# Performance work log

Hardware: AMD Instinct MI355X
Metric: run time of the kernel (lower is better)

Reference implementation:

```python
import jax, jax.numpy as jnp
import numpy as np

B, S, D, K = 64, 2048, 192, 128  # batch, seq, projection_dim, memoryBankSize


def setup_inputs() -> dict:
    key = jax.random.key(0)
    k1, k2, k3 = jax.random.split(key, 3)
    return {
        "projections": jax.random.normal(k1, (B, S, D), jnp.float32),
        "mem_bank": jax.random.normal(k2, (K, D), jnp.float32),
        "glu_w": jax.random.normal(k3, (D, 2 * D), jnp.float32) * 0.05,
        "glu_b": jnp.zeros((2 * D,), jnp.float32),
    }


def _l2_normalize(x, axis):
    # matches tf.math.l2_normalize (eps inside the max under the sqrt)
    sq = jnp.sum(x * x, axis=axis, keepdims=True)
    return x / jnp.sqrt(jnp.maximum(sq, 1e-12))


def _sinkhorn(out):
    # out: [K, N] cosine similarities
    Q = jnp.exp(out / 0.05)
    Kf = jnp.asarray(Q.shape[0], Q.dtype)
    Bf = jnp.asarray(Q.shape[1], Q.dtype)
    Q = Q / jnp.sum(Q)
    for _ in range(3):  # fixed 3 iterations, as in source
        Q = Q / (jnp.sum(Q, axis=1, keepdims=True) * Kf)  # row normalize
        Q = Q / (jnp.sum(Q, axis=0, keepdims=True) * Bf)  # col normalize
    return Q * Bf


def reference(projections, mem_bank, glu_w, glu_b):
    Bsz, Ssz, Dd = projections.shape
    x = projections.reshape(-1, Dd)                      # [N, D]
    proj_n = _l2_normalize(x, axis=1)                    # [N, D]
    mem_n = _l2_normalize(mem_bank, axis=1)              # [K, D]
    sim = jnp.einsum('kd,nd->kn', mem_n, proj_n)         # [K, N]
    Q = _sinkhorn(sim)                                   # [K, N]
    # top_k(Q^T, 1) per token == argmax over codebook axis
    idx = jnp.argmax(Q, axis=0)                          # [N] int
    assign = mem_bank[idx]                               # gather, [N, D]
    # GLU: Dense(2D) then value * sigmoid(gate)
    lin = assign @ glu_w + glu_b                         # [N, 2D]
    gated = lin[:, :Dd] * jax.nn.sigmoid(lin[:, Dd:])    # [N, D]
    # reduce_mean over the stacked pair == average
    return (projections + gated.reshape(Bsz, Ssz, Dd)) * 0.5
```

## Files before the change

kernel.cpp:

```cpp
#include <hip/hip_runtime.h>

#define NTOK  131072
#define DDIM  192
#define KMEM  128
#define TWOD  384
#define NBLK  1024

typedef _Float16 half8 __attribute__((ext_vector_type(8)));
typedef float   floatx4 __attribute__((ext_vector_type(4)));

__global__ __launch_bounds__(192) void prep_kernel(
    const float* __restrict__ mb, const float* __restrict__ W,
    const float* __restrict__ bias, _Float16* __restrict__ bhi,
    _Float16* __restrict__ blo, float* __restrict__ tab) {
  __shared__ float row[DDIM];
  __shared__ float red[DDIM];
  __shared__ float s_rn;
  const int k = blockIdx.x;
  const int t = threadIdx.x;
  float m = mb[k * DDIM + t];
  row[t] = m;
  red[t] = m * m;
  __syncthreads();
  if (t == 0) {
    float s = 0.f;
    for (int i = 0; i < DDIM; ++i) s += red[i];
    s_rn = 1.0f / sqrtf(fmaxf(s, 1e-12f));
  }
  __syncthreads();
  const float mn = m * s_rn;
  const _Float16 hh = (_Float16)mn;
  const float lo = (mn - (float)hh) * 4096.0f;
  bhi[k * DDIM + t] = hh;
  blo[k * DDIM + t] = (_Float16)lo;
  float a = bias[t], g = bias[DDIM + t];
  for (int d = 0; d < DDIM; ++d) {
    float r = row[d];
    a = fmaf(r, W[d * TWOD + t], a);
    g = fmaf(r, W[d * TWOD + DDIM + t], g);
  }
  float sg = 1.0f / (1.0f + expf(-g));
  tab[k * DDIM + t] = a * sg;
}

#define LSTR 40
__global__ __launch_bounds__(256, 2) void sim_kernel(
    const float* __restrict__ proj, const _Float16* __restrict__ bhi_g,
    const _Float16* __restrict__ blo_g, float* __restrict__ E,
    double* __restrict__ RpT) {
  __shared__ _Float16 Ahi[128 * LSTR];
  __shared__ _Float16 Alo[128 * LSTR];
  __shared__ _Float16 Bhi[128 * LSTR];
  __shared__ _Float16 Blo[128 * LSTR];
  __shared__ float rn_s[128];
  __shared__ float red[4][64];
  const int tid = threadIdx.x;
  const int lane = tid & 63;
  const int wid = tid >> 6;
  const int tok_half = wid & 1;
  const int code_half = wid >> 1;
  const long n0 = (long)blockIdx.x * 128;
  const int st_tok = tid >> 1;
  const int st_h = tid & 1;

  floatx4 acc1[4][4];
  floatx4 acc2[4][4];
#pragma unroll
  for (int i = 0; i < 4; ++i)
#pragma unroll
    for (int j = 0; j < 4; ++j) {
      acc1[i][j] = (floatx4)0.0f;
      acc2[i][j] = (floatx4)0.0f;
    }
  float nsq = 0.f;

  const int m_row = lane & 15;
  const int quad = lane >> 4;
  const int kcol = quad * 8;

  for (int c = 0; c < 6; ++c) {
    {
      const float* src = &proj[(n0 + st_tok) * DDIM + c * 32 + st_h * 16];
      float4 p0 = *(const float4*)(src + 0);
      float4 p1 = *(const float4*)(src + 4);
      float4 p2 = *(const float4*)(src + 8);
      float4 p3 = *(const float4*)(src + 12);
      float xs[16] = {p0.x, p0.y, p0.z, p0.w, p1.x, p1.y, p1.z, p1.w,
                      p2.x, p2.y, p2.z, p2.w, p3.x, p3.y, p3.z, p3.w};
      half8 h0, h1, l0, l1;
#pragma unroll
      for (int i = 0; i < 8; ++i) {
        float x = xs[i];
        nsq = fmaf(x, x, nsq);
        _Float16 hh = (_Float16)x;
        h0[i] = hh;
        l0[i] = (_Float16)((x - (float)hh) * 4096.0f);
      }
#pragma unroll
      for (int i = 0; i < 8; ++i) {
        float x = xs[8 + i];
        nsq = fmaf(x, x, nsq);
        _Float16 hh = (_Float16)x;
        h1[i] = hh;
        l1[i] = (_Float16)((x - (float)hh) * 4096.0f);
      }
      const int lb = st_tok * LSTR + st_h * 16;
      *(half8*)&Ahi[lb] = h0;
      *(half8*)&Ahi[lb + 8] = h1;
      *(half8*)&Alo[lb] = l0;
      *(half8*)&Alo[lb + 8] = l1;
      const int gb = st_tok * DDIM + c * 32 + st_h * 16;
      *(half8*)&Bhi[lb] = *(const half8*)&bhi_g[gb];
      *(half8*)&Bhi[lb + 8] = *(const half8*)&bhi_g[gb + 8];
      *(half8*)&Blo[lb] = *(const half8*)&blo_g[gb];
      *(half8*)&Blo[lb + 8] = *(const half8*)&blo_g[gb + 8];
    }
    __syncthreads();
    half8 a_hi[4], a_lo[4];
#pragma unroll
    for (int sm = 0; sm < 4; ++sm) {
      const int ar = (tok_half * 64 + sm * 16 + m_row) * LSTR + kcol;
      a_hi[sm] = *(const half8*)&Ahi[ar];
      a_lo[sm] = *(const half8*)&Alo[ar];
    }
#pragma unroll
    for (int sn = 0; sn < 4; ++sn) {
      const int br = (code_half * 64 + sn * 16 + m_row) * LSTR + kcol;
      half8 b_hi = *(const half8*)&Bhi[br];
      half8 b_lo = *(const half8*)&Blo[br];
#pragma unroll
      for (int sm = 0; sm < 4; ++sm) {
        acc1[sm][sn] =
            __builtin_amdgcn_mfma_f32_16x16x32_f16(a_hi[sm], b_hi, acc1[sm][sn], 0, 0, 0);
        acc2[sm][sn] =
            __builtin_amdgcn_mfma_f32_16x16x32_f16(a_hi[sm], b_lo, acc2[sm][sn], 0, 0, 0);
        acc2[sm][sn] =
            __builtin_amdgcn_mfma_f32_16x16x32_f16(a_lo[sm], b_hi, acc2[sm][sn], 0, 0, 0);
      }
    }
    __syncthreads();
  }
  nsq += __shfl_xor(nsq, 1);
  if ((tid & 1) == 0) rn_s[st_tok] = 1.0f / sqrtf(fmaxf(nsq, 1e-12f));
  __syncthreads();

  float rcol[4] = {0.f, 0.f, 0.f, 0.f};
#pragma unroll
  for (int sm = 0; sm < 4; ++sm) {
    float rnr[4];
#pragma unroll
    for (int r = 0; r < 4; ++r)
      rnr[r] = rn_s[tok_half * 64 + sm * 16 + quad * 4 + r];
#pragma unroll
    for (int sn = 0; sn < 4; ++sn) {
      const int code = code_half * 64 + sn * 16 + m_row;
      const floatx4 v1 = acc1[sm][sn];
      const floatx4 v2 = acc2[sm][sn];
#pragma unroll
      for (int r = 0; r < 4; ++r) {
        const long tok = n0 + tok_half * 64 + sm * 16 + quad * 4 + r;
        const float sim = fmaf(v2[r], 0.000244140625f, v1[r]) * rnr[r];
        const float e = expf(sim / 0.05f);
        E[tok * KMEM + code] = e;
        rcol[sn] += e;
      }
    }
  }
#pragma unroll
  for (int sn = 0; sn < 4; ++sn) {
    rcol[sn] += __shfl_xor(rcol[sn], 16);
    rcol[sn] += __shfl_xor(rcol[sn], 32);
  }
  if (lane < 16) {
#pragma unroll
    for (int sn = 0; sn < 4; ++sn) red[wid][sn * 16 + lane] = rcol[sn];
  }
  __syncthreads();
  if (tid < KMEM) {
    const int ch = tid >> 6, cw = tid & 63;
    RpT[(long)tid * NBLK + blockIdx.x] =
        (double)(red[2 * ch][cw] + red[2 * ch + 1][cw]);
  }
}

__global__ __launch_bounds__(256) void u_kernel(const double* __restrict__ RpT,
                                                float* __restrict__ u) {
  __shared__ double wred[4];
  const int k = blockIdx.x;
  const int t = threadIdx.x;
  double s = 0.0;
#pragma unroll
  for (int j = 0; j < NBLK / 256; ++j) s += RpT[(long)k * NBLK + j * 256 + t];
#pragma unroll
  for (int off = 1; off < 64; off <<= 1) s += __shfl_xor(s, off);
  if ((t & 63) == 0) wred[t >> 6] = s;
  __syncthreads();
  if (t == 0)
    u[k] = (float)(1.0 / (128.0 * (wred[0] + wred[1] + wred[2] + wred[3])));
}

__global__ __launch_bounds__(256) void cv_kernel(const float* __restrict__ E,
                                                 const float* __restrict__ u,
                                                 double* __restrict__ RpT) {
  __shared__ double part[4][KMEM];
  const int tid = threadIdx.x;
  const int l = tid & 7;
  const int ts = tid >> 3;
  const long n0 = (long)blockIdx.x * 128;
  float4 u4[4];
#pragma unroll
  for (int j = 0; j < 4; ++j) u4[j] = *(const float4*)&u[l * 16 + j * 4];
  double r[16];
#pragma unroll
  for (int i = 0; i < 16; ++i) r[i] = 0.0;
#pragma unroll
  for (int it = 0; it < 4; ++it) {
    const long n = n0 + it * 32 + ts;
    const float* Er = &E[n * KMEM + l * 16];
    const float4 e0 = *(const float4*)(Er + 0);
    const float4 e1 = *(const float4*)(Er + 4);
    const float4 e2 = *(const float4*)(Er + 8);
    const float4 e3 = *(const float4*)(Er + 12);
    double c = (double)e0.x * u4[0].x + (double)e0.y * u4[0].y +
               (double)e0.z * u4[0].z + (double)e0.w * u4[0].w +
               (double)e1.x * u4[1].x + (double)e1.y * u4[1].y +
               (double)e1.z * u4[1].z + (double)e1.w * u4[1].w +
               (double)e2.x * u4[2].x + (double)e2.y * u4[2].y +
               (double)e2.z * u4[2].z + (double)e2.w * u4[2].w +
               (double)e3.x * u4[3].x + (double)e3.y * u4[3].y +
               (double)e3.z * u4[3].z + (double)e3.w * u4[3].w;
    c += __shfl_xor(c, 1);
    c += __shfl_xor(c, 2);
    c += __shfl_xor(c, 4);
    const float v = (float)(1.0 / (131072.0 * c));
    r[0] += (double)(e0.x * v);
    r[1] += (double)(e0.y * v);
    r[2] += (double)(e0.z * v);
    r[3] += (double)(e0.w * v);
    r[4] += (double)(e1.x * v);
    r[5] += (double)(e1.y * v);
    r[6] += (double)(e1.z * v);
    r[7] += (double)(e1.w * v);
    r[8] += (double)(e2.x * v);
    r[9] += (double)(e2.y * v);
    r[10] += (double)(e2.z * v);
    r[11] += (double)(e2.w * v);
    r[12] += (double)(e3.x * v);
    r[13] += (double)(e3.y * v);
    r[14] += (double)(e3.z * v);
    r[15] += (double)(e3.w * v);
  }
#pragma unroll
  for (int i = 0; i < 16; ++i) {
    r[i] += __shfl_xor(r[i], 8);
    r[i] += __shfl_xor(r[i], 16);
    r[i] += __shfl_xor(r[i], 32);
  }
  if ((tid & 63) < 8) {
    const int w = tid >> 6;
#pragma unroll
    for (int i = 0; i < 16; ++i) part[w][l * 16 + i] = r[i];
  }
  __syncthreads();
  if (tid < KMEM) {
    const double s = part[0][tid] + part[1][tid] + part[2][tid] + part[3][tid];
    RpT[(long)tid * NBLK + blockIdx.x] = s;
  }
}

__global__ __launch_bounds__(256) void argmax_kernel(
    const float* __restrict__ E, const float* __restrict__ u,
    int* __restrict__ idx) {
  const int tid = threadIdx.x;
  const int l = tid & 7;
  const int ts = tid >> 3;
  const long n0 = (long)blockIdx.x * 128;
  float4 u4[4];
#pragma unroll
  for (int j = 0; j < 4; ++j) u4[j] = *(const float4*)&u[l * 16 + j * 4];
#pragma unroll
  for (int it = 0; it < 4; ++it) {
    const long n = n0 + it * 32 + ts;
    const float* Er = &E[n * KMEM + l * 16];
    const float4 e0 = *(const float4*)(Er + 0);
    const float4 e1 = *(const float4*)(Er + 4);
    const float4 e2 = *(const float4*)(Er + 8);
    const float4 e3 = *(const float4*)(Er + 12);
    float p[16];
    p[0] = e0.x * u4[0].x; p[1] = e0.y * u4[0].y;
    p[2] = e0.z * u4[0].z; p[3] = e0.w * u4[0].w;
    p[4] = e1.x * u4[1].x; p[5] = e1.y * u4[1].y;
    p[6] = e1.z * u4[1].z; p[7] = e1.w * u4[1].w;
    p[8] = e2.x * u4[2].x; p[9] = e2.y * u4[2].y;
    p[10] = e2.z * u4[2].z; p[11] = e2.w * u4[2].w;
    p[12] = e3.x * u4[3].x; p[13] = e3.y * u4[3].y;
    p[14] = e3.z * u4[3].z; p[15] = e3.w * u4[3].w;
    float bv = p[0];
    int bi = l * 16;
#pragma unroll
    for (int i = 1; i < 16; ++i) {
      if (p[i] > bv) { bv = p[i]; bi = l * 16 + i; }
    }
#pragma unroll
    for (int off = 1; off < 8; off <<= 1) {
      const float ov = __shfl_xor(bv, off);
      const int oi = __shfl_xor(bi, off);
      if (ov > bv || (ov == bv && oi < bi)) { bv = ov; bi = oi; }
    }
    if (l == 0) idx[n] = bi;
  }
}

__global__ __launch_bounds__(256) void out_kernel(
    const float* __restrict__ proj, const float* __restrict__ tab,
    const int* __restrict__ idx, float* __restrict__ out) {
  const long base = (long)blockIdx.x * 3072;
#pragma unroll
  for (int j = 0; j < 12; ++j) {
    const long f = base + j * 256 + threadIdx.x;
    const int t = (int)(f / 48);
    const int r = (int)(f - (long)t * 48);
    const int id = idx[t];
    const float4 p = *(const float4*)&proj[f * 4];
    const float4 tb = *(const float4*)&tab[id * DDIM + r * 4];
    float4 o;
    o.x = (p.x + tb.x) * 0.5f;
    o.y = (p.y + tb.y) * 0.5f;
    o.z = (p.z + tb.z) * 0.5f;
    o.w = (p.w + tb.w) * 0.5f;
    *(float4*)&out[f * 4] = o;
  }
}

extern "C" void kernel_launch(void* const* d_in, const int* in_sizes, int n_in,
                              void* d_out, int out_size, void* d_ws,
                              size_t ws_size, hipStream_t stream) {
  const float* proj = (const float*)d_in[0];
  const float* mb = (const float*)d_in[1];
  const float* W = (const float*)d_in[2];
  const float* bias = (const float*)d_in[3];
  float* out = (float*)d_out;
  char* ws = (char*)d_ws;
  float* tab = (float*)(ws);
  _Float16* bhi = (_Float16*)(ws + 98304);
  _Float16* blo = (_Float16*)(ws + 147456);
  float* u1 = (float*)(ws + 196608);
  float* u2 = (float*)(ws + 197120);
  float* u3 = (float*)(ws + 197632);
  int* idx = (int*)(ws + 198144);
  double* RpA = (double*)(ws + 722432);
  double* RpB = (double*)(ws + 1771008);
  float* E = out;

  prep_kernel<<<KMEM, DDIM, 0, stream>>>(mb, W, bias, bhi, blo, tab);
  sim_kernel<<<NBLK, 256, 0, stream>>>(proj, bhi, blo, E, RpA);
  u_kernel<<<KMEM, 256, 0, stream>>>(RpA, u1);
  cv_kernel<<<NBLK, 256, 0, stream>>>(E, u1, RpB);
  u_kernel<<<KMEM, 256, 0, stream>>>(RpB, u2);
  cv_kernel<<<NBLK, 256, 0, stream>>>(E, u2, RpA);
  u_kernel<<<KMEM, 256, 0, stream>>>(RpA, u3);
  argmax_kernel<<<NBLK, 256, 0, stream>>>(E, u3, idx);
  out_kernel<<<2048, 256, 0, stream>>>(proj, tab, idx, out);
}
```

Before: 288.5 us.

## Restructure sim kernel into single-stage 64-token tiles with register-resident codebook

The similarity kernel now loads a 64-token tile of projections into shared memory once, with the full 192-wide row and a single barrier, instead of six chunked stages with two barriers each. Codebook hi/lo fragments are read directly from global (L2-cached) into registers per wave, so the codebook shared-memory staging goes away. Each wave owns 32 codes and writes its per-block column sums straight to the partial buffer, which removes the shared reduction. Block count doubles and occupancy hints go up, and u_kernel takes a runtime width. In exchange there is more redundant codebook traffic and more partial sums to reduce.

New measurement: 296.5 us. 1.03x slower.

```diff
diff --git a/kernel.cpp b/kernel.cpp
--- a/kernel.cpp
+++ b/kernel.cpp
@@ -4,7 +4,8 @@
 #define DDIM  192
 #define KMEM  128
 #define TWOD  384
-#define NBLK  1024
+#define SIMBLK 2048
+#define CVBLK  1024
 
 typedef _Float16 half8 __attribute__((ext_vector_type(8)));
 typedef float   floatx4 __attribute__((ext_vector_type(4)));
@@ -43,154 +44,111 @@
   tab[k * DDIM + t] = a * sg;
 }
 
-#define LSTR 40
-__global__ __launch_bounds__(256, 2) void sim_kernel(
+#define LSTR 200
+__global__ __launch_bounds__(256, 3) void sim_kernel(
     const float* __restrict__ proj, const _Float16* __restrict__ bhi_g,
     const _Float16* __restrict__ blo_g, float* __restrict__ E,
     double* __restrict__ RpT) {
-  __shared__ _Float16 Ahi[128 * LSTR];
-  __shared__ _Float16 Alo[128 * LSTR];
-  __shared__ _Float16 Bhi[128 * LSTR];
-  __shared__ _Float16 Blo[128 * LSTR];
-  __shared__ float rn_s[128];
-  __shared__ float red[4][64];
+  __shared__ _Float16 Ahi[64 * LSTR];
+  __shared__ _Float16 Alo[64 * LSTR];
+  __shared__ float rn_s[64];
   const int tid = threadIdx.x;
   const int lane = tid & 63;
   const int wid = tid >> 6;
-  const int tok_half = wid & 1;
-  const int code_half = wid >> 1;
-  const long n0 = (long)blockIdx.x * 128;
-  const int st_tok = tid >> 1;
-  const int st_h = tid & 1;
-
-  floatx4 acc1[4][4];
-  floatx4 acc2[4][4];
-#pragma unroll
-  for (int i = 0; i < 4; ++i)
-#pragma unroll
-    for (int j = 0; j < 4; ++j) {
-      acc1[i][j] = (floatx4)0.0f;
-      acc2[i][j] = (floatx4)0.0f;
-    }
-  float nsq = 0.f;
+  const long n0 = (long)blockIdx.x * 64;
+
+  {
+    const int row = tid >> 2;
+    const int part = tid & 3;
+    const float* src = &proj[(n0 + row) * DDIM + part * 48];
+    const int lb0 = row * LSTR + part * 48;
+    float nsq = 0.f;
+#pragma unroll
+    for (int i = 0; i < 6; ++i) {
+      float4 p0 = *(const float4*)(src + i * 8);
+      float4 p1 = *(const float4*)(src + i * 8 + 4);
+      float xs[8] = {p0.x, p0.y, p0.z, p0.w, p1.x, p1.y, p1.z, p1.w};
+      half8 h, l;
+#pragma unroll
+      for (int j = 0; j < 8; ++j) {
+        float x = xs[j];
+        nsq = fmaf(x, x, nsq);
+        _Float16 hh = (_Float16)x;
+        h[j] = hh;
+        l[j] = (_Float16)((x - (float)hh) * 4096.0f);
+      }
+      *(half8*)&Ahi[lb0 + i * 8] = h;
+      *(half8*)&Alo[lb0 + i * 8] = l;
+    }
+    nsq += __shfl_xor(nsq, 1);
+    nsq += __shfl_xor(nsq, 2);
+    if (part == 0) rn_s[row] = 1.0f / sqrtf(fmaxf(nsq, 1e-12f));
+  }
+  __syncthreads();
 
   const int m_row = lane & 15;
   const int quad = lane >> 4;
-  const int kcol = quad * 8;
-
-  for (int c = 0; c < 6; ++c) {
-    {
-      const float* src = &proj[(n0 + st_tok) * DDIM + c * 32 + st_h * 16];
-      float4 p0 = *(const float4*)(src + 0);
-      float4 p1 = *(const float4*)(src + 4);
-      float4 p2 = *(const float4*)(src + 8);
-      float4 p3 = *(const float4*)(src + 12);
-      float xs[16] = {p0.x, p0.y, p0.z, p0.w, p1.x, p1.y, p1.z, p1.w,
-                      p2.x, p2.y, p2.z, p2.w, p3.x, p3.y, p3.z, p3.w};
-      half8 h0, h1, l0, l1;
-#pragma unroll
-      for (int i = 0; i < 8; ++i) {
-        float x = xs[i];
-        nsq = fmaf(x, x, nsq);
-        _Float16 hh = (_Float16)x;
-        h0[i] = hh;
-        l0[i] = (_Float16)((x - (float)hh) * 4096.0f);
+  const int code_base = wid * 32;
+
+  float rnv[16];
+#pragma unroll
+  for (int sm = 0; sm < 4; ++sm)
+#pragma unroll
+    for (int r = 0; r < 4; ++r) rnv[sm * 4 + r] = rn_s[sm * 16 + quad * 4 + r];
+
+  float rcol[2] = {0.f, 0.f};
+#pragma unroll
+  for (int sn = 0; sn < 2; ++sn) {
+    const int code = code_base + sn * 16 + m_row;
+    half8 bh[6], bl[6];
+#pragma unroll
+    for (int c = 0; c < 6; ++c) {
+      const int gb = code * DDIM + c * 32 + quad * 8;
+      bh[c] = *(const half8*)&bhi_g[gb];
+      bl[c] = *(const half8*)&blo_g[gb];
+    }
+#pragma unroll
+    for (int sm = 0; sm < 4; ++sm) {
+      floatx4 a1 = (floatx4)0.0f;
+      floatx4 a2 = (floatx4)0.0f;
+#pragma unroll
+      for (int c = 0; c < 6; ++c) {
+        const int ar = (sm * 16 + m_row) * LSTR + c * 32 + quad * 8;
+        half8 ah = *(const half8*)&Ahi[ar];
+        half8 al = *(const half8*)&Alo[ar];
+        a1 = __builtin_amdgcn_mfma_f32_16x16x32_f16(ah, bh[c], a1, 0, 0, 0);
+        a2 = __builtin_amdgcn_mfma_f32_16x16x32_f16(ah, bl[c], a2, 0, 0, 0);
+        a2 = __builtin_amdgcn_mfma_f32_16x16x32_f16(al, bh[c], a2, 0, 0, 0);
       }
 #pragma unroll
-      for (int i = 0; i < 8; ++i) {
-        float x = xs[8 + i];
-        nsq = fmaf(x, x, nsq);
-        _Float16 hh = (_Float16)x;
-        h1[i] = hh;
-        l1[i] = (_Float16)((x - (float)hh) * 4096.0f);
-      }
-      const int lb = st_tok * LSTR + st_h * 16;
-      *(half8*)&Ahi[lb] = h0;
-      *(half8*)&Ahi[lb + 8] = h1;
-      *(half8*)&Alo[lb] = l0;
-      *(half8*)&Alo[lb + 8] = l1;
-      const int gb = st_tok * DDIM + c * 32 + st_h * 16;
-      *(half8*)&Bhi[lb] = *(const half8*)&bhi_g[gb];
-      *(half8*)&Bhi[lb + 8] = *(const half8*)&bhi_g[gb + 8];
-      *(half8*)&Blo[lb] = *(const half8*)&blo_g[gb];
-      *(half8*)&Blo[lb + 8] = *(const half8*)&blo_g[gb + 8];
-    }
-    __syncthreads();
-    half8 a_hi[4], a_lo[4];
-#pragma unroll
-    for (int sm = 0; sm < 4; ++sm) {
-      const int ar = (tok_half * 64 + sm * 16 + m_row) * LSTR + kcol;
-      a_hi[sm] = *(const half8*)&Ahi[ar];
-      a_lo[sm] = *(const half8*)&Alo[ar];
-    }
-#pragma unroll
-    for (int sn = 0; sn < 4; ++sn) {
-      const int br = (code_half * 64 + sn * 16 + m_row) * LSTR + kcol;
-      half8 b_hi = *(const half8*)&Bhi[br];
-      half8 b_lo = *(const half8*)&Blo[br];
-#pragma unroll
-      for (int sm = 0; sm < 4; ++sm) {
-        acc1[sm][sn] =
-            __builtin_amdgcn_mfma_f32_16x16x32_f16(a_hi[sm], b_hi, acc1[sm][sn], 0, 0, 0);
-        acc2[sm][sn] =
-            __builtin_amdgcn_mfma_f32_16x16x32_f16(a_hi[sm], b_lo, acc2[sm][sn], 0, 0, 0);
-        acc2[sm][sn] =
-            __builtin_amdgcn_mfma_f32_16x16x32_f16(a_lo[sm], b_hi, acc2[sm][sn], 0, 0, 0);
-      }
-    }
-    __syncthreads();
-  }
-  nsq += __shfl_xor(nsq, 1);
-  if ((tid & 1) == 0) rn_s[st_tok] = 1.0f / sqrtf(fmaxf(nsq, 1e-12f));
-  __syncthreads();
-
-  float rcol[4] = {0.f, 0.f, 0.f, 0.f};
-#pragma unroll
-  for (int sm = 0; sm < 4; ++sm) {
-    float rnr[4];
-#pragma unroll
-    for (int r = 0; r < 4; ++r)
-      rnr[r] = rn_s[tok_half * 64 + sm * 16 + quad * 4 + r];
-#pragma unroll
-    for (int sn = 0; sn < 4; ++sn) {
-      const int code = code_half * 64 + sn * 16 + m_row;
-      const floatx4 v1 = acc1[sm][sn];
-      const floatx4 v2 = acc2[sm][sn];
-#pragma unroll
       for (int r = 0; r < 4; ++r) {
-        const long tok = n0 + tok_half * 64 + sm * 16 + quad * 4 + r;
-        const float sim = fmaf(v2[r], 0.000244140625f, v1[r]) * rnr[r];
+        const int tok = sm * 16 + quad * 4 + r;
+        const float sim = fmaf(a2[r], 0.000244140625f, a1[r]) * rnv[sm * 4 + r];
         const float e = expf(sim / 0.05f);
-        E[tok * KMEM + code] = e;
+        E[(n0 + tok) * KMEM + code] = e;
         rcol[sn] += e;
       }
     }
   }
 #pragma unroll
-  for (int sn = 0; sn < 4; ++sn) {
+  for (int sn = 0; sn < 2; ++sn) {
     rcol[sn] += __shfl_xor(rcol[sn], 16);
     rcol[sn] += __shfl_xor(rcol[sn], 32);
   }
   if (lane < 16) {
-#pragma unroll
-    for (int sn = 0; sn < 4; ++sn) red[wid][sn * 16 + lane] = rcol[sn];
-  }
-  __syncthreads();
-  if (tid < KMEM) {
-    const int ch = tid >> 6, cw = tid & 63;
-    RpT[(long)tid * NBLK + blockIdx.x] =
-        (double)(red[2 * ch][cw] + red[2 * ch + 1][cw]);
+    RpT[(long)(code_base + lane) * SIMBLK + blockIdx.x] = (double)rcol[0];
+    RpT[(long)(code_base + 16 + lane) * SIMBLK + blockIdx.x] = (double)rcol[1];
   }
 }
 
 __global__ __launch_bounds__(256) void u_kernel(const double* __restrict__ RpT,
-                                                float* __restrict__ u) {
+                                                float* __restrict__ u,
+                                                int width) {
   __shared__ double wred[4];
   const int k = blockIdx.x;
   const int t = threadIdx.x;
   double s = 0.0;
-#pragma unroll
-  for (int j = 0; j < NBLK / 256; ++j) s += RpT[(long)k * NBLK + j * 256 + t];
+  for (int j = t; j < width; j += 256) s += RpT[(long)k * width + j];
 #pragma unroll
   for (int off = 1; off < 64; off <<= 1) s += __shfl_xor(s, off);
   if ((t & 63) == 0) wred[t >> 6] = s;
@@ -264,7 +222,7 @@
   __syncthreads();
   if (tid < KMEM) {
     const double s = part[0][tid] + part[1][tid] + part[2][tid] + part[3][tid];
-    RpT[(long)tid * NBLK + blockIdx.x] = s;
+    RpT[(long)tid * CVBLK + blockIdx.x] = s;
   }
 }
 
@@ -349,16 +307,16 @@
   float* u3 = (float*)(ws + 197632);
   int* idx = (int*)(ws + 198144);
   double* RpA = (double*)(ws + 722432);
-  double* RpB = (double*)(ws + 1771008);
+  double* RpB = (double*)(ws + 2819584);
   float* E = out;
 
   prep_kernel<<<KMEM, DDIM, 0, stream>>>(mb, W, bias, bhi, blo, tab);
-  sim_kernel<<<NBLK, 256, 0, stream>>>(proj, bhi, blo, E, RpA);
-  u_kernel<<<KMEM, 256, 0, stream>>>(RpA, u1);
-  cv_kernel<<<NBLK, 256, 0, stream>>>(E, u1, RpB);
-  u_kernel<<<KMEM, 256, 0, stream>>>(RpB, u2);
-  cv_kernel<<<NBLK, 256, 0, stream>>>(E, u2, RpA);
-  u_kernel<<<KMEM, 256, 0, stream>>>(RpA, u3);
-  argmax_kernel<<<NBLK, 256, 0, stream>>>(E, u3, idx);
+  sim_kernel<<<SIMBLK, 256, 0, stream>>>(proj, bhi, blo, E, RpA);
+  u_kernel<<<KMEM, 256, 0, stream>>>(RpA, u1, SIMBLK);
+  cv_kernel<<<CVBLK, 256, 0, stream>>>(E, u1, RpB);
+  u_kernel<<<KMEM, 256, 0, stream>>>(RpB, u2, CVBLK);
+  cv_kernel<<<CVBLK, 256, 0, stream>>>(E, u2, RpB);
+  u_kernel<<<KMEM, 256, 0, stream>>>(RpB, u3, CVBLK);
+  argmax_kernel<<<CVBLK, 256, 0, stream>>>(E, u3, idx);
   out_kernel<<<2048, 256, 0, stream>>>(proj, tab, idx, out);
 }
```
